# Kernel optimization log

Hardware: AMD Instinct MI355X
Metric: run time of the kernel (lower is better)

The kernel has to match this reference:

```python
import jax, jax.numpy as jnp
import numpy as np

N_QUBITS = 12
N_LAYERS = 6
BATCH = 1024


def setup_inputs() -> dict:
    key = jax.random.key(0)
    k1, k2, k3, k4 = jax.random.split(key, 4)
    x = jax.random.normal(k1, (BATCH, N_QUBITS), dtype=jnp.float32)
    weights = jax.random.normal(k2, (N_LAYERS, N_QUBITS, 3), dtype=jnp.float32)
    head_w = jax.random.normal(k3, (2, 1), dtype=jnp.float32)
    head_b = jax.random.normal(k4, (2,), dtype=jnp.float32)
    return {"x": x, "weights": weights, "head_w": head_w, "head_b": head_b}


def _apply_1q(state, U, q):
    # state: (B, 2**n) complex64; U: (2,2) or (B,2,2)
    B = state.shape[0]
    st = state.reshape(B, 1 << q, 2, -1)  # isolate qubit q
    if U.ndim == 2:
        new = jnp.einsum('ij,bajc->baic', U, st)
    else:
        new = jnp.einsum('bij,bajc->baic', U, st)
    return new.reshape(B, -1)


def _cnot_adj(state, q):
    # CNOT with control q, target q+1 (adjacent)
    B = state.shape[0]
    st = state.reshape(B, 1 << q, 2, 2, -1)
    new = jnp.concatenate([st[:, :, :1], st[:, :, 1:, ::-1]], axis=2)
    return new.reshape(B, -1)


def _rot_mat(phi, theta, omega):
    # PennyLane Rot = RZ(omega) RY(theta) RZ(phi)
    c = jnp.cos(0.5 * theta)
    s = jnp.sin(0.5 * theta)
    ep = jnp.exp(-0.5j * (phi + omega))
    em = jnp.exp(-0.5j * (phi - omega))
    row0 = jnp.stack([ep * c, -jnp.conj(em) * s])
    row1 = jnp.stack([em * s, jnp.conj(ep) * c])
    return jnp.stack([row0, row1]).astype(jnp.complex64)


def _layer(state, wl, n):
    # wl: (n, 3) Rot params for this layer, then CNOT cascade
    for q in range(n):
        state = _apply_1q(state, _rot_mat(wl[q, 0], wl[q, 1], wl[q, 2]), q)
    for q in range(n - 1):
        state = _cnot_adj(state, q)
    return state


def _circuit(x, weights):
    B, n = x.shape
    state = jnp.zeros((B, 1 << n), jnp.complex64).at[:, 0].set(1.0 + 0.0j)
    # AngleEmbedding: RX(x_q) on qubit q (batched gates)
    for q in range(n):
        h = 0.5 * x[:, q]
        c, s = jnp.cos(h), jnp.sin(h)
        U = jnp.stack([jnp.stack([c, -1j * s], -1),
                       jnp.stack([-1j * s, c], -1)], -2).astype(jnp.complex64)
        state = _apply_1q(state, U, q)
    state = jax.lax.scan(lambda s, wl: (_layer(s, wl, n), None), state, weights)[0]
    # <Z_0>
    p = jnp.abs(state.reshape(B, 2, -1)) ** 2
    return (p[:, 0].sum(-1) - p[:, 1].sum(-1)).astype(jnp.float32)


def reference(x, weights, head_w, head_b):
    z = _circuit(x, weights)            # (B,) expectation values
    q_out = z[:, None]                  # (B, 1)
    return q_out @ head_w.T + head_b    # Linear(1, 2) -> (B, 2)
```

## Files before the change

### kernel.cpp

```cpp
#include <hip/hip_runtime.h>

#define NQ 12
#define NSTATE (1 << NQ)
#define TPB 256


typedef float f4 __attribute__((ext_vector_type(4)));

struct A2 { float ar, ai, br, bi; };

__device__ __forceinline__ float RL(float v, int idx) {
    return __int_as_float(__builtin_amdgcn_readlane(__float_as_int(v), idx));
}

__device__ __forceinline__ void bf2(A2& s0, A2& s1,
                                    float A, float B, float C, float D) {
    float n0r, n0i, n1r, n1i;
    n0r = fmaf(A, s0.ar, fmaf( B, s0.ai, fmaf(-C, s1.ar,  D * s1.ai)));
    n0i = fmaf(A, s0.ai, fmaf(-B, s0.ar, fmaf(-C, s1.ai, -D * s1.ar)));
    n1r = fmaf(C, s0.ar, fmaf( D, s0.ai, fmaf( A, s1.ar, -B * s1.ai)));
    n1i = fmaf(C, s0.ai, fmaf(-D, s0.ar, fmaf( A, s1.ai,  B * s1.ar)));
    s0.ar = n0r; s0.ai = n0i; s1.ar = n1r; s1.ai = n1i;
    n0r = fmaf(A, s0.br, fmaf( B, s0.bi, fmaf(-C, s1.br,  D * s1.bi)));
    n0i = fmaf(A, s0.bi, fmaf(-B, s0.br, fmaf(-C, s1.bi, -D * s1.br)));
    n1r = fmaf(C, s0.br, fmaf( D, s0.bi, fmaf( A, s1.br, -B * s1.bi)));
    n1i = fmaf(C, s0.bi, fmaf(-D, s0.br, fmaf( A, s1.bi,  B * s1.br)));
    s0.br = n0r; s0.bi = n0i; s1.br = n1r; s1.bi = n1i;
}

#define BF(i,j) bf2(a##i, a##j, A, B, C, D)
#define PK0 BF(0,1); BF(2,3); BF(4,5); BF(6,7); \
            BF(8,9); BF(10,11); BF(12,13); BF(14,15);
#define PK1 BF(0,2); BF(1,3); BF(4,6); BF(5,7); \
            BF(8,10); BF(9,11); BF(12,14); BF(13,15);
#define PK2 BF(0,4); BF(1,5); BF(2,6); BF(3,7); \
            BF(8,12); BF(9,13); BF(10,14); BF(11,15);
#define PK3 BF(0,8); BF(1,9); BF(2,10); BF(3,11); \
            BF(4,12); BF(5,13); BF(6,14); BF(7,15);
#define GATE(qq, P) { const int gi = gb + (qq); \
    const float A = RL(gA, gi), B = RL(gB, gi), \
                C = RL(gC, gi), D = RL(gD, gi); P }

#define LDS4(off) (*(f4*)((char*)st + (off)))
#define LD1(r, ADR) { f4 v = LDS4(ADR(r)); \
    a##r.ar = v.x; a##r.ai = v.y; a##r.br = v.z; a##r.bi = v.w; }
#define ST1(r, ADR) { f4 v = {a##r.ar, a##r.ai, a##r.br, a##r.bi}; \
    LDS4(ADR(r)) = v; }
#define LD16(ADR) { LD1(0,ADR) LD1(1,ADR) LD1(2,ADR) LD1(3,ADR) \
                    LD1(4,ADR) LD1(5,ADR) LD1(6,ADR) LD1(7,ADR) \
                    LD1(8,ADR) LD1(9,ADR) LD1(10,ADR) LD1(11,ADR) \
                    LD1(12,ADR) LD1(13,ADR) LD1(14,ADR) LD1(15,ADR) }
#define ST16(ADR) { ST1(0,ADR) ST1(1,ADR) ST1(2,ADR) ST1(3,ADR) \
                    ST1(4,ADR) ST1(5,ADR) ST1(6,ADR) ST1(7,ADR) \
                    ST1(8,ADR) ST1(9,ADR) ST1(10,ADR) ST1(11,ADR) \
                    ST1(12,ADR) ST1(13,ADR) ST1(14,ADR) ST1(15,ADR) }

#define ADRA(r)   (ptAb + ((r) << 12))
#define ADRB(r)   (ptBb ^ (((r) << 8) ^ ((r) << 4)))
#define ADRC(r)   (ptCb ^ ((r) << 4))
#define GINV4(r)  ((r) ^ ((r) >> 1) ^ ((r) >> 2) ^ ((r) >> 3))
#define ADRCS(r)  (ptCSb ^ (GINV4(r) << 4))

#define CM(n, xr, xi, yr, yi) \
    const float n##r = fmaf(xr, yr, -(xi) * (yi)); \
    const float n##i = fmaf(xr, yi,  (xi) * (yr));
#define GCONST(q) const float A##q = RL(gA, q), B##q = RL(gB, q), \
                              C##q = RL(gC, q), D##q = RL(gD, q);
#define VQDEF(q) \
    const float v##q##0r = fmaf(A##q, c##q, -(D##q) * s##q); \
    const float v##q##0i = fmaf(-(B##q), c##q,  (C##q) * s##q); \
    const float v##q##1r = fmaf(C##q, c##q,  (B##q) * s##q); \
    const float v##q##1i = fmaf(-(D##q), c##q, -(A##q) * s##q);
#define WSEL(q, b) \
    const float w##q##r = (tj & (1 << (b))) ? v##q##1r : v##q##0r; \
    const float w##q##i = (tj & (1 << (b))) ? v##q##1i : v##q##0i;
#define SETAMP(g, rp, mm, RE, IM) \
    a##g.RE = fmaf(mm##r, Q##rp##r, -(mm##i) * Q##rp##i); \
    a##g.IM = fmaf(mm##r, Q##rp##i,  (mm##i) * Q##rp##r);

__global__ __launch_bounds__(TPB) void qsim_kernel(
    const float* __restrict__ x,
    const float* __restrict__ w,
    const float* __restrict__ hw,
    const float* __restrict__ hb,
    float* __restrict__ out)
{
    __shared__ f4 st[NSTATE];

    const int t    = threadIdx.x;
    const int lane = t & 63;
    const int e0   = blockIdx.x * 2;

    float gA, gB, gC, gD;
    {
        const float* wl = w + lane * 3;
        float phi = wl[0], th = wl[1], om = wl[2];
        float c, s, ca, sa, cb, sb;
        __sincosf(0.5f * th, &s, &c);
        __sincosf(0.5f * (phi + om), &sa, &ca);
        __sincosf(0.5f * (phi - om), &sb, &cb);
        gA = c * ca; gB = c * sa; gC = s * cb; gD = s * sb;
    }

    const int ptAb  = (t ^ (t >> 4)) << 4;
    const int ptBb  = ((((t & 0xF0) << 4) | (t & 0x0F))) << 4;
    const int ptCb  = (((t << 4) ^ (t & 0x0F))) << 4;
    int gv = t << 4;
    gv ^= gv >> 1; gv ^= gv >> 2; gv ^= gv >> 4; gv ^= gv >> 8; gv &= 0xFFF;
    const int ptCSb = (gv ^ ((gv >> 4) & 0xF)) << 4;

    A2 a0, a1, a2, a3, a4, a5, a6, a7,
       a8, a9, a10, a11, a12, a13, a14, a15;

    #pragma unroll 1
    for (int k = 0; k < 4; ++k) {
        const int gb = (k + 1) * 12;

        if (k == 0) {
            const int tj = t ^ (t >> 1);
            const int t7 = (t >> 7) & 1;
            GCONST(0)  GCONST(1)  GCONST(2)  GCONST(3)
            GCONST(4)  GCONST(5)  GCONST(6)  GCONST(7)
            GCONST(8)  GCONST(9)  GCONST(10) GCONST(11)
            {
                const float* xe = x + e0 * NQ;
                float c0,s0,c1,s1,c2,s2,c3,s3,c4,s4,c5,s5;
                float c6,s6,c7,s7,c8,s8,c9,s9,c10,s10,c11,s11;
                #define EMB(q) __sincosf(0.5f * xe[q], &s##q, &c##q);
                EMB(0) EMB(1) EMB(2) EMB(3) EMB(4)  EMB(5)
                EMB(6) EMB(7) EMB(8) EMB(9) EMB(10) EMB(11)
                VQDEF(5)  WSEL(5,6)  VQDEF(6)  WSEL(6,5)
                VQDEF(7)  WSEL(7,4)  VQDEF(8)  WSEL(8,3)
                VQDEF(9)  WSEL(9,2)  VQDEF(10) WSEL(10,1)
                VQDEF(11) WSEL(11,0)
                CM(m56, w5r, w5i, w6r, w6i)   CM(m78, w7r, w7i, w8r, w8i)
                CM(m9A, w9r, w9i, w10r, w10i)
                CM(mP, m56r, m56i, m78r, m78i) CM(mQ, m9Ar, m9Ai, w11r, w11i)
                CM(mL, mPr, mPi, mQr, mQi)
                VQDEF(4)
                const float w4ar = t7 ? v41r : v40r, w4ai = t7 ? v41i : v40i;
                const float w4br = t7 ? v40r : v41r, w4bi = t7 ? v40i : v41i;
                CM(Pa, mLr, mLi, w4ar, w4ai)   CM(Pb, mLr, mLi, w4br, w4bi)
                VQDEF(3)
                CM(T00, Par, Pai, v30r, v30i)  CM(T01, Par, Pai, v31r, v31i)
                CM(T10, Pbr, Pbi, v31r, v31i)  CM(T11, Pbr, Pbi, v30r, v30i)
                VQDEF(0) VQDEF(1) VQDEF(2)
                CM(H0, v00r, v00i, v10r, v10i) CM(H1, v00r, v00i, v11r, v11i)
                CM(H2, v01r, v01i, v10r, v10i) CM(H3, v01r, v01i, v11r, v11i)
                CM(Q0, H0r, H0i, v20r, v20i)   CM(Q1, H0r, H0i, v21r, v21i)
                CM(Q2, H1r, H1i, v20r, v20i)   CM(Q3, H1r, H1i, v21r, v21i)
                CM(Q4, H2r, H2i, v20r, v20i)   CM(Q5, H2r, H2i, v21r, v21i)
                CM(Q6, H3r, H3i, v20r, v20i)   CM(Q7, H3r, H3i, v21r, v21i)
                SETAMP(0,0,T00,ar,ai)  SETAMP(1,0,T10,ar,ai)
                SETAMP(2,1,T01,ar,ai)  SETAMP(3,1,T11,ar,ai)
                SETAMP(4,3,T00,ar,ai)  SETAMP(5,3,T10,ar,ai)
                SETAMP(6,2,T01,ar,ai)  SETAMP(7,2,T11,ar,ai)
                SETAMP(8,6,T00,ar,ai)  SETAMP(9,6,T10,ar,ai)
                SETAMP(10,7,T01,ar,ai) SETAMP(11,7,T11,ar,ai)
                SETAMP(12,5,T00,ar,ai) SETAMP(13,5,T10,ar,ai)
                SETAMP(14,4,T01,ar,ai) SETAMP(15,4,T11,ar,ai)
            }
            {
                const float* xe = x + (e0 + 1) * NQ;
                float c0,s0,c1,s1,c2,s2,c3,s3,c4,s4,c5,s5;
                float c6,s6,c7,s7,c8,s8,c9,s9,c10,s10,c11,s11;
                EMB(0) EMB(1) EMB(2) EMB(3) EMB(4)  EMB(5)
                EMB(6) EMB(7) EMB(8) EMB(9) EMB(10) EMB(11)
                #undef EMB
                VQDEF(5)  WSEL(5,6)  VQDEF(6)  WSEL(6,5)
                VQDEF(7)  WSEL(7,4)  VQDEF(8)  WSEL(8,3)
                VQDEF(9)  WSEL(9,2)  VQDEF(10) WSEL(10,1)
                VQDEF(11) WSEL(11,0)
                CM(m56, w5r, w5i, w6r, w6i)   CM(m78, w7r, w7i, w8r, w8i)
                CM(m9A, w9r, w9i, w10r, w10i)
                CM(mP, m56r, m56i, m78r, m78i) CM(mQ, m9Ar, m9Ai, w11r, w11i)
                CM(mL, mPr, mPi, mQr, mQi)
                VQDEF(4)
                const float w4ar = t7 ? v41r : v40r, w4ai = t7 ? v41i : v40i;
                const float w4br = t7 ? v40r : v41r, w4bi = t7 ? v40i : v41i;
                CM(Pa, mLr, mLi, w4ar, w4ai)   CM(Pb, mLr, mLi, w4br, w4bi)
                VQDEF(3)
                CM(T00, Par, Pai, v30r, v30i)  CM(T01, Par, Pai, v31r, v31i)
                CM(T10, Pbr, Pbi, v31r, v31i)  CM(T11, Pbr, Pbi, v30r, v30i)
                VQDEF(0) VQDEF(1) VQDEF(2)
                CM(H0, v00r, v00i, v10r, v10i) CM(H1, v00r, v00i, v11r, v11i)
                CM(H2, v01r, v01i, v10r, v10i) CM(H3, v01r, v01i, v11r, v11i)
                CM(Q0, H0r, H0i, v20r, v20i)   CM(Q1, H0r, H0i, v21r, v21i)
                CM(Q2, H1r, H1i, v20r, v20i)   CM(Q3, H1r, H1i, v21r, v21i)
                CM(Q4, H2r, H2i, v20r, v20i)   CM(Q5, H2r, H2i, v21r, v21i)
                CM(Q6, H3r, H3i, v20r, v20i)   CM(Q7, H3r, H3i, v21r, v21i)
                SETAMP(0,0,T00,br,bi)  SETAMP(1,0,T10,br,bi)
                SETAMP(2,1,T01,br,bi)  SETAMP(3,1,T11,br,bi)
                SETAMP(4,3,T00,br,bi)  SETAMP(5,3,T10,br,bi)
                SETAMP(6,2,T01,br,bi)  SETAMP(7,2,T11,br,bi)
                SETAMP(8,6,T00,br,bi)  SETAMP(9,6,T10,br,bi)
                SETAMP(10,7,T01,br,bi) SETAMP(11,7,T11,br,bi)
                SETAMP(12,5,T00,br,bi) SETAMP(13,5,T10,br,bi)
                SETAMP(14,4,T01,br,bi) SETAMP(15,4,T11,br,bi)
            }
        } else {
            LD16(ADRA)
        }
        GATE(3, PK0) GATE(2, PK1) GATE(1, PK2) GATE(0, PK3)
        ST16(ADRA)
        __syncthreads();

        LD16(ADRB)
        GATE(7, PK0) GATE(6, PK1) GATE(5, PK2) GATE(4, PK3)
        ST16(ADRB)
        __syncthreads();

        LD16(ADRC)
        GATE(11, PK0) GATE(10, PK1) GATE(9, PK2) GATE(8, PK3)
        __syncthreads();
        ST16(ADRCS)
        __syncthreads();
    }

    LD16(ADRA)
    {
        const float A = RL(gA, 60), B = RL(gB, 60),
                    C = RL(gC, 60), D = RL(gD, 60);
        bf2(a0, a8,  A, B, C, D); bf2(a1, a9,  A, B, C, D);
        bf2(a2, a10, A, B, C, D); bf2(a3, a11, A, B, C, D);
        bf2(a4, a12, A, B, C, D); bf2(a5, a13, A, B, C, D);
        bf2(a6, a14, A, B, C, D); bf2(a7, a15, A, B, C, D);
    }

    float za = 0.0f, zb = 0.0f;
    za += a0.ar*a0.ar + a0.ai*a0.ai;    zb += a0.br*a0.br + a0.bi*a0.bi;
    za += a1.ar*a1.ar + a1.ai*a1.ai;    zb += a1.br*a1.br + a1.bi*a1.bi;
    za += a2.ar*a2.ar + a2.ai*a2.ai;    zb += a2.br*a2.br + a2.bi*a2.bi;
    za += a3.ar*a3.ar + a3.ai*a3.ai;    zb += a3.br*a3.br + a3.bi*a3.bi;
    za += a4.ar*a4.ar + a4.ai*a4.ai;    zb += a4.br*a4.br + a4.bi*a4.bi;
    za += a5.ar*a5.ar + a5.ai*a5.ai;    zb += a5.br*a5.br + a5.bi*a5.bi;
    za += a6.ar*a6.ar + a6.ai*a6.ai;    zb += a6.br*a6.br + a6.bi*a6.bi;
    za += a7.ar*a7.ar + a7.ai*a7.ai;    zb += a7.br*a7.br + a7.bi*a7.bi;
    za -= a8.ar*a8.ar + a8.ai*a8.ai;    zb -= a8.br*a8.br + a8.bi*a8.bi;
    za -= a9.ar*a9.ar + a9.ai*a9.ai;    zb -= a9.br*a9.br + a9.bi*a9.bi;
    za -= a10.ar*a10.ar + a10.ai*a10.ai; zb -= a10.br*a10.br + a10.bi*a10.bi;
    za -= a11.ar*a11.ar + a11.ai*a11.ai; zb -= a11.br*a11.br + a11.bi*a11.bi;
    za -= a12.ar*a12.ar + a12.ai*a12.ai; zb -= a12.br*a12.br + a12.bi*a12.bi;
    za -= a13.ar*a13.ar + a13.ai*a13.ai; zb -= a13.br*a13.br + a13.bi*a13.bi;
    za -= a14.ar*a14.ar + a14.ai*a14.ai; zb -= a14.br*a14.br + a14.bi*a14.bi;
    za -= a15.ar*a15.ar + a15.ai*a15.ai; zb -= a15.br*a15.br + a15.bi*a15.bi;

    #pragma unroll
    for (int off = 32; off >= 1; off >>= 1) {
        za += __shfl_down(za, off);
        zb += __shfl_down(zb, off);
    }

    __syncthreads();
    float* red = (float*)st;
    if (lane == 0) { red[t >> 6] = za; red[4 + (t >> 6)] = zb; }
    __syncthreads();

    if (t == 0) {
        float zta = red[0] + red[1] + red[2] + red[3];
        float ztb = red[4] + red[5] + red[6] + red[7];
        out[2 * e0 + 0] = zta * hw[0] + hb[0];
        out[2 * e0 + 1] = zta * hw[1] + hb[1];
        out[2 * e0 + 2] = ztb * hw[0] + hb[0];
        out[2 * e0 + 3] = ztb * hw[1] + hb[1];
    }
}

extern "C" void kernel_launch(void* const* d_in, const int* in_sizes, int n_in,
                              void* d_out, int out_size, void* d_ws, size_t ws_size,
                              hipStream_t stream) {
    const float* x  = (const float*)d_in[0];
    const float* w  = (const float*)d_in[1];
    const float* hw = (const float*)d_in[2];
    const float* hb = (const float*)d_in[3];
    float* out = (float*)d_out;
    const int B = in_sizes[0] / NQ;
    qsim_kernel<<<B / 2, TPB, 0, stream>>>(x, w, hw, hb, out);
}
```

Baseline: 39.56 us.

## Process one batch element per block instead of two interleaved

Each block now simulates a single batch element's 4096-amplitude state held as float2 in LDS, instead of two elements packed into float4. The grid doubles to B blocks and LDS use per block halves, so more blocks can be resident per CU and each thread carries half the registers. In exchange, the per-block overhead (gate-constant setup, barriers, reductions) is paid twice as often. LDS accesses drop from 16-byte to 8-byte width, which may change bank-conflict behaviour under the existing swizzle.

After: 40.42 us. 1.02x slower.

```diff
diff --git a/kernel.cpp b/kernel.cpp
--- a/kernel.cpp
+++ b/kernel.cpp
@@ -5,30 +5,20 @@
 #define TPB 256
 
 
-typedef float f4 __attribute__((ext_vector_type(4)));
-
-struct A2 { float ar, ai, br, bi; };
-
 __device__ __forceinline__ float RL(float v, int idx) {
     return __int_as_float(__builtin_amdgcn_readlane(__float_as_int(v), idx));
 }
 
-__device__ __forceinline__ void bf2(A2& s0, A2& s1,
+__device__ __forceinline__ void bf1(float2& s0, float2& s1,
                                     float A, float B, float C, float D) {
-    float n0r, n0i, n1r, n1i;
-    n0r = fmaf(A, s0.ar, fmaf( B, s0.ai, fmaf(-C, s1.ar,  D * s1.ai)));
-    n0i = fmaf(A, s0.ai, fmaf(-B, s0.ar, fmaf(-C, s1.ai, -D * s1.ar)));
-    n1r = fmaf(C, s0.ar, fmaf( D, s0.ai, fmaf( A, s1.ar, -B * s1.ai)));
-    n1i = fmaf(C, s0.ai, fmaf(-D, s0.ar, fmaf( A, s1.ai,  B * s1.ar)));
-    s0.ar = n0r; s0.ai = n0i; s1.ar = n1r; s1.ai = n1i;
-    n0r = fmaf(A, s0.br, fmaf( B, s0.bi, fmaf(-C, s1.br,  D * s1.bi)));
-    n0i = fmaf(A, s0.bi, fmaf(-B, s0.br, fmaf(-C, s1.bi, -D * s1.br)));
-    n1r = fmaf(C, s0.br, fmaf( D, s0.bi, fmaf( A, s1.br, -B * s1.bi)));
-    n1i = fmaf(C, s0.bi, fmaf(-D, s0.br, fmaf( A, s1.bi,  B * s1.br)));
-    s0.br = n0r; s0.bi = n0i; s1.br = n1r; s1.bi = n1i;
-}
-
-#define BF(i,j) bf2(a##i, a##j, A, B, C, D)
+    float n0x = fmaf(A, s0.x, fmaf( B, s0.y, fmaf(-C, s1.x,  D * s1.y)));
+    float n0y = fmaf(A, s0.y, fmaf(-B, s0.x, fmaf(-C, s1.y, -D * s1.x)));
+    float n1x = fmaf(C, s0.x, fmaf( D, s0.y, fmaf( A, s1.x, -B * s1.y)));
+    float n1y = fmaf(C, s0.y, fmaf(-D, s0.x, fmaf( A, s1.y,  B * s1.x)));
+    s0 = make_float2(n0x, n0y); s1 = make_float2(n1x, n1y);
+}
+
+#define BF(i,j) bf1(a##i, a##j, A, B, C, D)
 #define PK0 BF(0,1); BF(2,3); BF(4,5); BF(6,7); \
             BF(8,9); BF(10,11); BF(12,13); BF(14,15);
 #define PK1 BF(0,2); BF(1,3); BF(4,6); BF(5,7); \
@@ -41,11 +31,9 @@
     const float A = RL(gA, gi), B = RL(gB, gi), \
                 C = RL(gC, gi), D = RL(gD, gi); P }
 
-#define LDS4(off) (*(f4*)((char*)st + (off)))
-#define LD1(r, ADR) { f4 v = LDS4(ADR(r)); \
-    a##r.ar = v.x; a##r.ai = v.y; a##r.br = v.z; a##r.bi = v.w; }
-#define ST1(r, ADR) { f4 v = {a##r.ar, a##r.ai, a##r.br, a##r.bi}; \
-    LDS4(ADR(r)) = v; }
+#define LDS2(off) (*(float2*)((char*)st + (off)))
+#define LD1(r, ADR) a##r = LDS2(ADR(r));
+#define ST1(r, ADR) LDS2(ADR(r)) = a##r;
 #define LD16(ADR) { LD1(0,ADR) LD1(1,ADR) LD1(2,ADR) LD1(3,ADR) \
                     LD1(4,ADR) LD1(5,ADR) LD1(6,ADR) LD1(7,ADR) \
                     LD1(8,ADR) LD1(9,ADR) LD1(10,ADR) LD1(11,ADR) \
@@ -55,11 +43,11 @@
                     ST1(8,ADR) ST1(9,ADR) ST1(10,ADR) ST1(11,ADR) \
                     ST1(12,ADR) ST1(13,ADR) ST1(14,ADR) ST1(15,ADR) }
 
-#define ADRA(r)   (ptAb + ((r) << 12))
-#define ADRB(r)   (ptBb ^ (((r) << 8) ^ ((r) << 4)))
-#define ADRC(r)   (ptCb ^ ((r) << 4))
+#define ADRA(r)   (ptAb + ((r) << 11))
+#define ADRB(r)   (ptBb ^ (((r) << 7) ^ ((r) << 3)))
+#define ADRC(r)   (ptCb ^ ((r) << 3))
 #define GINV4(r)  ((r) ^ ((r) >> 1) ^ ((r) >> 2) ^ ((r) >> 3))
-#define ADRCS(r)  (ptCSb ^ (GINV4(r) << 4))
+#define ADRCS(r)  (ptCSb ^ (GINV4(r) << 3))
 
 #define CM(n, xr, xi, yr, yi) \
     const float n##r = fmaf(xr, yr, -(xi) * (yi)); \
@@ -74,9 +62,9 @@
 #define WSEL(q, b) \
     const float w##q##r = (tj & (1 << (b))) ? v##q##1r : v##q##0r; \
     const float w##q##i = (tj & (1 << (b))) ? v##q##1i : v##q##0i;
-#define SETAMP(g, rp, mm, RE, IM) \
-    a##g.RE = fmaf(mm##r, Q##rp##r, -(mm##i) * Q##rp##i); \
-    a##g.IM = fmaf(mm##r, Q##rp##i,  (mm##i) * Q##rp##r);
+#define SETAMP(g, rp, mm) \
+    a##g = make_float2(fmaf(mm##r, Q##rp##r, -(mm##i) * Q##rp##i), \
+                       fmaf(mm##r, Q##rp##i,  (mm##i) * Q##rp##r));
 
 __global__ __launch_bounds__(TPB) void qsim_kernel(
     const float* __restrict__ x,
@@ -85,11 +73,11 @@
     const float* __restrict__ hb,
     float* __restrict__ out)
 {
-    __shared__ f4 st[NSTATE];
+    __shared__ float2 st[NSTATE];
 
     const int t    = threadIdx.x;
     const int lane = t & 63;
-    const int e0   = blockIdx.x * 2;
+    const int e    = blockIdx.x;
 
     float gA, gB, gC, gD;
     {
@@ -102,15 +90,15 @@
         gA = c * ca; gB = c * sa; gC = s * cb; gD = s * sb;
     }
 
-    const int ptAb  = (t ^ (t >> 4)) << 4;
-    const int ptBb  = ((((t & 0xF0) << 4) | (t & 0x0F))) << 4;
-    const int ptCb  = (((t << 4) ^ (t & 0x0F))) << 4;
+    const int ptAb  = (t ^ (t >> 4)) << 3;
+    const int ptBb  = ((((t & 0xF0) << 4) | (t & 0x0F))) << 3;
+    const int ptCb  = (((t << 4) ^ (t & 0x0F))) << 3;
     int gv = t << 4;
     gv ^= gv >> 1; gv ^= gv >> 2; gv ^= gv >> 4; gv ^= gv >> 8; gv &= 0xFFF;
-    const int ptCSb = (gv ^ ((gv >> 4) & 0xF)) << 4;
-
-    A2 a0, a1, a2, a3, a4, a5, a6, a7,
-       a8, a9, a10, a11, a12, a13, a14, a15;
+    const int ptCSb = (gv ^ ((gv >> 4) & 0xF)) << 3;
+
+    float2 a0, a1, a2, a3, a4, a5, a6, a7,
+           a8, a9, a10, a11, a12, a13, a14, a15;
 
     #pragma unroll 1
     for (int k = 0; k < 4; ++k) {
@@ -122,82 +110,43 @@
             GCONST(0)  GCONST(1)  GCONST(2)  GCONST(3)
             GCONST(4)  GCONST(5)  GCONST(6)  GCONST(7)
             GCONST(8)  GCONST(9)  GCONST(10) GCONST(11)
-            {
-                const float* xe = x + e0 * NQ;
-                float c0,s0,c1,s1,c2,s2,c3,s3,c4,s4,c5,s5;
-                float c6,s6,c7,s7,c8,s8,c9,s9,c10,s10,c11,s11;
-                #define EMB(q) __sincosf(0.5f * xe[q], &s##q, &c##q);
-                EMB(0) EMB(1) EMB(2) EMB(3) EMB(4)  EMB(5)
-                EMB(6) EMB(7) EMB(8) EMB(9) EMB(10) EMB(11)
-                VQDEF(5)  WSEL(5,6)  VQDEF(6)  WSEL(6,5)
-                VQDEF(7)  WSEL(7,4)  VQDEF(8)  WSEL(8,3)
-                VQDEF(9)  WSEL(9,2)  VQDEF(10) WSEL(10,1)
-                VQDEF(11) WSEL(11,0)
-                CM(m56, w5r, w5i, w6r, w6i)   CM(m78, w7r, w7i, w8r, w8i)
-                CM(m9A, w9r, w9i, w10r, w10i)
-                CM(mP, m56r, m56i, m78r, m78i) CM(mQ, m9Ar, m9Ai, w11r, w11i)
-                CM(mL, mPr, mPi, mQr, mQi)
-                VQDEF(4)
-                const float w4ar = t7 ? v41r : v40r, w4ai = t7 ? v41i : v40i;
-                const float w4br = t7 ? v40r : v41r, w4bi = t7 ? v40i : v41i;
-                CM(Pa, mLr, mLi, w4ar, w4ai)   CM(Pb, mLr, mLi, w4br, w4bi)
-                VQDEF(3)
-                CM(T00, Par, Pai, v30r, v30i)  CM(T01, Par, Pai, v31r, v31i)
-                CM(T10, Pbr, Pbi, v31r, v31i)  CM(T11, Pbr, Pbi, v30r, v30i)
-                VQDEF(0) VQDEF(1) VQDEF(2)
-                CM(H0, v00r, v00i, v10r, v10i) CM(H1, v00r, v00i, v11r, v11i)
-                CM(H2, v01r, v01i, v10r, v10i) CM(H3, v01r, v01i, v11r, v11i)
-                CM(Q0, H0r, H0i, v20r, v20i)   CM(Q1, H0r, H0i, v21r, v21i)
-                CM(Q2, H1r, H1i, v20r, v20i)   CM(Q3, H1r, H1i, v21r, v21i)
-                CM(Q4, H2r, H2i, v20r, v20i)   CM(Q5, H2r, H2i, v21r, v21i)
-                CM(Q6, H3r, H3i, v20r, v20i)   CM(Q7, H3r, H3i, v21r, v21i)
-                SETAMP(0,0,T00,ar,ai)  SETAMP(1,0,T10,ar,ai)
-                SETAMP(2,1,T01,ar,ai)  SETAMP(3,1,T11,ar,ai)
-                SETAMP(4,3,T00,ar,ai)  SETAMP(5,3,T10,ar,ai)
-                SETAMP(6,2,T01,ar,ai)  SETAMP(7,2,T11,ar,ai)
-                SETAMP(8,6,T00,ar,ai)  SETAMP(9,6,T10,ar,ai)
-                SETAMP(10,7,T01,ar,ai) SETAMP(11,7,T11,ar,ai)
-                SETAMP(12,5,T00,ar,ai) SETAMP(13,5,T10,ar,ai)
-                SETAMP(14,4,T01,ar,ai) SETAMP(15,4,T11,ar,ai)
-            }
-            {
-                const float* xe = x + (e0 + 1) * NQ;
-                float c0,s0,c1,s1,c2,s2,c3,s3,c4,s4,c5,s5;
-                float c6,s6,c7,s7,c8,s8,c9,s9,c10,s10,c11,s11;
-                EMB(0) EMB(1) EMB(2) EMB(3) EMB(4)  EMB(5)
-                EMB(6) EMB(7) EMB(8) EMB(9) EMB(10) EMB(11)
-                #undef EMB
-                VQDEF(5)  WSEL(5,6)  VQDEF(6)  WSEL(6,5)
-                VQDEF(7)  WSEL(7,4)  VQDEF(8)  WSEL(8,3)
-                VQDEF(9)  WSEL(9,2)  VQDEF(10) WSEL(10,1)
-                VQDEF(11) WSEL(11,0)
-                CM(m56, w5r, w5i, w6r, w6i)   CM(m78, w7r, w7i, w8r, w8i)
-                CM(m9A, w9r, w9i, w10r, w10i)
-                CM(mP, m56r, m56i, m78r, m78i) CM(mQ, m9Ar, m9Ai, w11r, w11i)
-                CM(mL, mPr, mPi, mQr, mQi)
-                VQDEF(4)
-                const float w4ar = t7 ? v41r : v40r, w4ai = t7 ? v41i : v40i;
-                const float w4br = t7 ? v40r : v41r, w4bi = t7 ? v40i : v41i;
-                CM(Pa, mLr, mLi, w4ar, w4ai)   CM(Pb, mLr, mLi, w4br, w4bi)
-                VQDEF(3)
-                CM(T00, Par, Pai, v30r, v30i)  CM(T01, Par, Pai, v31r, v31i)
-                CM(T10, Pbr, Pbi, v31r, v31i)  CM(T11, Pbr, Pbi, v30r, v30i)
-                VQDEF(0) VQDEF(1) VQDEF(2)
-                CM(H0, v00r, v00i, v10r, v10i) CM(H1, v00r, v00i, v11r, v11i)
-                CM(H2, v01r, v01i, v10r, v10i) CM(H3, v01r, v01i, v11r, v11i)
-                CM(Q0, H0r, H0i, v20r, v20i)   CM(Q1, H0r, H0i, v21r, v21i)
-                CM(Q2, H1r, H1i, v20r, v20i)   CM(Q3, H1r, H1i, v21r, v21i)
-                CM(Q4, H2r, H2i, v20r, v20i)   CM(Q5, H2r, H2i, v21r, v21i)
-                CM(Q6, H3r, H3i, v20r, v20i)   CM(Q7, H3r, H3i, v21r, v21i)
-                SETAMP(0,0,T00,br,bi)  SETAMP(1,0,T10,br,bi)
-                SETAMP(2,1,T01,br,bi)  SETAMP(3,1,T11,br,bi)
-                SETAMP(4,3,T00,br,bi)  SETAMP(5,3,T10,br,bi)
-                SETAMP(6,2,T01,br,bi)  SETAMP(7,2,T11,br,bi)
-                SETAMP(8,6,T00,br,bi)  SETAMP(9,6,T10,br,bi)
-                SETAMP(10,7,T01,br,bi) SETAMP(11,7,T11,br,bi)
-                SETAMP(12,5,T00,br,bi) SETAMP(13,5,T10,br,bi)
-                SETAMP(14,4,T01,br,bi) SETAMP(15,4,T11,br,bi)
-            }
+            const float* xe = x + e * NQ;
+            float c0,s0,c1,s1,c2,s2,c3,s3,c4,s4,c5,s5;
+            float c6,s6,c7,s7,c8,s8,c9,s9,c10,s10,c11,s11;
+            #define EMB(q) __sincosf(0.5f * xe[q], &s##q, &c##q);
+            EMB(0) EMB(1) EMB(2) EMB(3) EMB(4)  EMB(5)
+            EMB(6) EMB(7) EMB(8) EMB(9) EMB(10) EMB(11)
+            #undef EMB
+            VQDEF(5)  WSEL(5,6)  VQDEF(6)  WSEL(6,5)
+            VQDEF(7)  WSEL(7,4)  VQDEF(8)  WSEL(8,3)
+            VQDEF(9)  WSEL(9,2)  VQDEF(10) WSEL(10,1)
+            VQDEF(11) WSEL(11,0)
+            CM(m56, w5r, w5i, w6r, w6i)   CM(m78, w7r, w7i, w8r, w8i)
+            CM(m9A, w9r, w9i, w10r, w10i)
+            CM(mP, m56r, m56i, m78r, m78i) CM(mQ, m9Ar, m9Ai, w11r, w11i)
+            CM(mL, mPr, mPi, mQr, mQi)
+            VQDEF(4)
+            const float w4ar = t7 ? v41r : v40r, w4ai = t7 ? v41i : v40i;
+            const float w4br = t7 ? v40r : v41r, w4bi = t7 ? v40i : v41i;
+            CM(Pa, mLr, mLi, w4ar, w4ai)   CM(Pb, mLr, mLi, w4br, w4bi)
+            VQDEF(3)
+            CM(T00, Par, Pai, v30r, v30i)  CM(T01, Par, Pai, v31r, v31i)
+            CM(T10, Pbr, Pbi, v31r, v31i)  CM(T11, Pbr, Pbi, v30r, v30i)
+            VQDEF(0) VQDEF(1) VQDEF(2)
+            CM(H0, v00r, v00i, v10r, v10i) CM(H1, v00r, v00i, v11r, v11i)
+            CM(H2, v01r, v01i, v10r, v10i) CM(H3, v01r, v01i, v11r, v11i)
+            CM(Q0, H0r, H0i, v20r, v20i)   CM(Q1, H0r, H0i, v21r, v21i)
+            CM(Q2, H1r, H1i, v20r, v20i)   CM(Q3, H1r, H1i, v21r, v21i)
+            CM(Q4, H2r, H2i, v20r, v20i)   CM(Q5, H2r, H2i, v21r, v21i)
+            CM(Q6, H3r, H3i, v20r, v20i)   CM(Q7, H3r, H3i, v21r, v21i)
+            SETAMP(0,0,T00)  SETAMP(1,0,T10)
+            SETAMP(2,1,T01)  SETAMP(3,1,T11)
+            SETAMP(4,3,T00)  SETAMP(5,3,T10)
+            SETAMP(6,2,T01)  SETAMP(7,2,T11)
+            SETAMP(8,6,T00)  SETAMP(9,6,T10)
+            SETAMP(10,7,T01) SETAMP(11,7,T11)
+            SETAMP(12,5,T00) SETAMP(13,5,T10)
+            SETAMP(14,4,T01) SETAMP(15,4,T11)
         } else {
             LD16(ADRA)
         }
@@ -221,48 +170,35 @@
     {
         const float A = RL(gA, 60), B = RL(gB, 60),
                     C = RL(gC, 60), D = RL(gD, 60);
-        bf2(a0, a8,  A, B, C, D); bf2(a1, a9,  A, B, C, D);
-        bf2(a2, a10, A, B, C, D); bf2(a3, a11, A, B, C, D);
-        bf2(a4, a12, A, B, C, D); bf2(a5, a13, A, B, C, D);
-        bf2(a6, a14, A, B, C, D); bf2(a7, a15, A, B, C, D);
-    }
-
-    float za = 0.0f, zb = 0.0f;
-    za += a0.ar*a0.ar + a0.ai*a0.ai;    zb += a0.br*a0.br + a0.bi*a0.bi;
-    za += a1.ar*a1.ar + a1.ai*a1.ai;    zb += a1.br*a1.br + a1.bi*a1.bi;
-    za += a2.ar*a2.ar + a2.ai*a2.ai;    zb += a2.br*a2.br + a2.bi*a2.bi;
-    za += a3.ar*a3.ar + a3.ai*a3.ai;    zb += a3.br*a3.br + a3.bi*a3.bi;
-    za += a4.ar*a4.ar + a4.ai*a4.ai;    zb += a4.br*a4.br + a4.bi*a4.bi;
-    za += a5.ar*a5.ar + a5.ai*a5.ai;    zb += a5.br*a5.br + a5.bi*a5.bi;
-    za += a6.ar*a6.ar + a6.ai*a6.ai;    zb += a6.br*a6.br + a6.bi*a6.bi;
-    za += a7.ar*a7.ar + a7.ai*a7.ai;    zb += a7.br*a7.br + a7.bi*a7.bi;
-    za -= a8.ar*a8.ar + a8.ai*a8.ai;    zb -= a8.br*a8.br + a8.bi*a8.bi;
-    za -= a9.ar*a9.ar + a9.ai*a9.ai;    zb -= a9.br*a9.br + a9.bi*a9.bi;
-    za -= a10.ar*a10.ar + a10.ai*a10.ai; zb -= a10.br*a10.br + a10.bi*a10.bi;
-    za -= a11.ar*a11.ar + a11.ai*a11.ai; zb -= a11.br*a11.br + a11.bi*a11.bi;
-    za -= a12.ar*a12.ar + a12.ai*a12.ai; zb -= a12.br*a12.br + a12.bi*a12.bi;
-    za -= a13.ar*a13.ar + a13.ai*a13.ai; zb -= a13.br*a13.br + a13.bi*a13.bi;
-    za -= a14.ar*a14.ar + a14.ai*a14.ai; zb -= a14.br*a14.br + a14.bi*a14.bi;
-    za -= a15.ar*a15.ar + a15.ai*a15.ai; zb -= a15.br*a15.br + a15.bi*a15.bi;
+        bf1(a0, a8,  A, B, C, D); bf1(a1, a9,  A, B, C, D);
+        bf1(a2, a10, A, B, C, D); bf1(a3, a11, A, B, C, D);
+        bf1(a4, a12, A, B, C, D); bf1(a5, a13, A, B, C, D);
+        bf1(a6, a14, A, B, C, D); bf1(a7, a15, A, B, C, D);
+    }
+
+    float za = 0.0f;
+    za += a0.x*a0.x + a0.y*a0.y;    za += a1.x*a1.x + a1.y*a1.y;
+    za += a2.x*a2.x + a2.y*a2.y;    za += a3.x*a3.x + a3.y*a3.y;
+    za += a4.x*a4.x + a4.y*a4.y;    za += a5.x*a5.x + a5.y*a5.y;
+    za += a6.x*a6.x + a6.y*a6.y;    za += a7.x*a7.x + a7.y*a7.y;
+    za -= a8.x*a8.x + a8.y*a8.y;    za -= a9.x*a9.x + a9.y*a9.y;
+    za -= a10.x*a10.x + a10.y*a10.y; za -= a11.x*a11.x + a11.y*a11.y;
+    za -= a12.x*a12.x + a12.y*a12.y; za -= a13.x*a13.x + a13.y*a13.y;
+    za -= a14.x*a14.x + a14.y*a14.y; za -= a15.x*a15.x + a15.y*a15.y;
 
     #pragma unroll
-    for (int off = 32; off >= 1; off >>= 1) {
+    for (int off = 32; off >= 1; off >>= 1)
         za += __shfl_down(za, off);
-        zb += __shfl_down(zb, off);
-    }
 
     __syncthreads();
     float* red = (float*)st;
-    if (lane == 0) { red[t >> 6] = za; red[4 + (t >> 6)] = zb; }
+    if (lane == 0) red[t >> 6] = za;
     __syncthreads();
 
     if (t == 0) {
-        float zta = red[0] + red[1] + red[2] + red[3];
-        float ztb = red[4] + red[5] + red[6] + red[7];
-        out[2 * e0 + 0] = zta * hw[0] + hb[0];
-        out[2 * e0 + 1] = zta * hw[1] + hb[1];
-        out[2 * e0 + 2] = ztb * hw[0] + hb[0];
-        out[2 * e0 + 3] = ztb * hw[1] + hb[1];
+        float zt = red[0] + red[1] + red[2] + red[3];
+        out[2 * e + 0] = zt * hw[0] + hb[0];
+        out[2 * e + 1] = zt * hw[1] + hb[1];
     }
 }
 
@@ -275,5 +211,5 @@
     const float* hb = (const float*)d_in[3];
     float* out = (float*)d_out;
     const int B = in_sizes[0] / NQ;
-    qsim_kernel<<<B / 2, TPB, 0, stream>>>(x, w, hw, hb, out);
-}
+    qsim_kernel<<<B, TPB, 0, stream>>>(x, w, hw, hb, out);
+}
```
